# Kernel optimization log

Hardware: AMD Instinct MI355X
Metric: run time of the kernel (lower is better)

## Reference

```python
import jax, jax.numpy as jnp
import numpy as np

KNOTS = 17

def _buffers(dtype=jnp.float32):
    t = jnp.linspace(0.0, 3.0, KNOTS, dtype=dtype)
    dt = 3.0 / (KNOTS - 1)
    w = jnp.full((KNOTS,), 2.0 * dt, dtype=dtype).at[0].set(dt).at[-1].set(dt)
    phi = jnp.exp(-jnp.square(t) / 2.0)
    return t, phi, w * phi


def setup_inputs() -> dict:
    key = jax.random.key(0)
    k1, k2 = jax.random.split(key)
    T, B, D, P = 32, 64, 256, 1024
    proj = jax.random.normal(k1, (T, B, D), dtype=jnp.float32)
    A = jax.random.normal(k2, (D, P), dtype=jnp.float32)
    return {"proj": proj, "A": A}


def reference(proj, A):
    t, phi, weights = _buffers(proj.dtype)
    # column-normalize random projection directions (matches A.div_(norm.clamp_min))
    A = A / jnp.maximum(jnp.linalg.norm(A, axis=0, keepdims=True), 1e-12)
    B = proj.shape[-2]
    # (T, B, P) projections, broadcast against knots -> (T, B, P, K)
    x_t = (proj @ A)[..., None] * t
    # empirical characteristic function averaged over batch dim B (dim -3)
    cos_mean = jnp.cos(x_t).mean(axis=-3)  # (T, P, K)
    sin_mean = jnp.sin(x_t).mean(axis=-3)  # (T, P, K)
    err = jnp.square(cos_mean - phi) + jnp.square(sin_mean)
    statistic = (err @ weights) * B  # (T, P)
    return statistic.mean()
```

## Files before the change

kernel.cpp:

```cpp
#include <hip/hip_runtime.h>

#define T_DIM 32
#define B_DIM 64
#define D_DIM 256
#define P_DIM 1024
#define NK    17
#define DT    0.1875f
#define NBLK  512

__global__ __launch_bounds__(512) void sig_main_kernel(const float* __restrict__ proj,
                                                       const float* __restrict__ A,
                                                       float* __restrict__ partials) {
  __shared__ float smem[16384];
  const int tid  = threadIdx.x;
  const int lane = tid & 63;
  const int wave = tid >> 6;
  const int p0   = blockIdx.x * 64;
  const int t    = blockIdx.y;

  float4* s4 = (float4*)smem;
  float4* p4 = (float4*)(smem + 8192);

  float xacc[8];
#pragma unroll
  for (int j = 0; j < 8; ++j) xacc[j] = 0.f;
  float nacc = 0.f;

  const float4* Ag = (const float4*)(A + p0);
  const float4* Pg = (const float4*)(proj + (size_t)t * B_DIM * D_DIM);

  for (int dc = 0; dc < D_DIM; dc += 128) {
#pragma unroll
    for (int r = 0; r < 4; ++r) {
      int i = tid + r * 512;
      int da = i >> 4, ca = i & 15;
      s4[i] = Ag[(dc + da) * (P_DIM / 4) + ca];
      int bp = i >> 5, cp = i & 31;
      p4[i] = Pg[(size_t)bp * (D_DIM / 4) + dc / 4 + cp];
    }
    __syncthreads();

    const float4* prow = p4 + wave * 8 * 32;
#pragma unroll 2
    for (int ds4 = 0; ds4 < 32; ++ds4) {
      int dd = ds4 * 4;
      float a0 = smem[(dd + 0) * 64 + lane];
      float a1 = smem[(dd + 1) * 64 + lane];
      float a2 = smem[(dd + 2) * 64 + lane];
      float a3 = smem[(dd + 3) * 64 + lane];
      nacc = fmaf(a0, a0, nacc);
      nacc = fmaf(a1, a1, nacc);
      nacc = fmaf(a2, a2, nacc);
      nacc = fmaf(a3, a3, nacc);
#pragma unroll
      for (int j = 0; j < 8; ++j) {
        float4 pj = prow[j * 32 + ds4];
        xacc[j] = fmaf(pj.x, a0, xacc[j]);
        xacc[j] = fmaf(pj.y, a1, xacc[j]);
        xacc[j] = fmaf(pj.z, a2, xacc[j]);
        xacc[j] = fmaf(pj.w, a3, xacc[j]);
      }
    }
    __syncthreads();
  }

  const float inv = rsqrtf(fmaxf(nacc, 1e-24f));
  float cs[NK], ss[NK];
#pragma unroll
  for (int k = 1; k < NK; ++k) { cs[k] = 0.f; ss[k] = 0.f; }

#pragma unroll
  for (int j = 0; j < 8; ++j) {
    float th = xacc[j] * inv * DT;
    float s1, c1;
    __sincosf(th, &s1, &c1);
    float twoc = 2.f * c1;
    float ckm1 = 1.f, skm1 = 0.f;
    float ck = c1, sk = s1;
    cs[1] += c1;
    ss[1] += s1;
#pragma unroll
    for (int k = 2; k < NK; ++k) {
      float cn = fmaf(twoc, ck, -ckm1);
      float sn = fmaf(twoc, sk, -skm1);
      cs[k] += cn;
      ss[k] += sn;
      ckm1 = ck; skm1 = sk; ck = cn; sk = sn;
    }
  }

#pragma unroll
  for (int k = 1; k < NK; ++k) {
    int k1 = k - 1;
    smem[k1 * 512 + wave * 64 + lane]        = cs[k];
    smem[8192 + k1 * 512 + wave * 64 + lane] = ss[k];
  }
  __syncthreads();

  float part = 0.f;
#pragma unroll
  for (int r = 0; r < 2; ++r) {
    int e  = tid + r * 512;
    int k1 = e >> 6;
    int pl = e & 63;
    const float* bc = &smem[k1 * 512 + pl];
    const float* bs = &smem[8192 + k1 * 512 + pl];
    float C = 0.f, S = 0.f;
#pragma unroll
    for (int w = 0; w < 8; ++w) { C += bc[w * 64]; S += bs[w * 64]; }
    float cm  = C * (1.f / 64.f);
    float sm  = S * (1.f / 64.f);
    float tk  = (float)(k1 + 1) * DT;
    float phi = __expf(-0.5f * tk * tk);
    float wk  = ((k1 == NK - 2) ? DT : 2.f * DT) * phi;
    float dc  = cm - phi;
    part = fmaf(wk, fmaf(dc, dc, sm * sm), part);
  }
  part *= (1.f / 512.f);

#pragma unroll
  for (int off = 32; off > 0; off >>= 1)
    part += __shfl_down(part, off, 64);
  __syncthreads();
  if (lane == 0) smem[wave] = part;
  __syncthreads();
  if (tid == 0) {
    float s = 0.f;
#pragma unroll
    for (int w = 0; w < 8; ++w) s += smem[w];
    partials[blockIdx.y * 16 + blockIdx.x] = s;
  }
}

__global__ __launch_bounds__(256) void sig_finalize_kernel(const float* __restrict__ partials,
                                                           float* __restrict__ out) {
  __shared__ float red[4];
  const int tid  = threadIdx.x;
  const int lane = tid & 63;
  const int wave = tid >> 6;
  float v = partials[tid] + partials[tid + 256];
#pragma unroll
  for (int off = 32; off > 0; off >>= 1)
    v += __shfl_down(v, off, 64);
  if (lane == 0) red[wave] = v;
  __syncthreads();
  if (tid == 0) out[0] = red[0] + red[1] + red[2] + red[3];
}

extern "C" void kernel_launch(void* const* d_in, const int* in_sizes, int n_in,
                              void* d_out, int out_size, void* d_ws, size_t ws_size,
                              hipStream_t stream) {
  const float* proj = (const float*)d_in[0];
  const float* A    = (const float*)d_in[1];
  float* partials   = (float*)d_ws;
  float* out        = (float*)d_out;

  sig_main_kernel<<<dim3(16, 32), dim3(512), 0, stream>>>(proj, A, partials);
  sig_finalize_kernel<<<dim3(1), dim3(256), 0, stream>>>(partials, out);
}
```

Before: 86.39 us.

## Stage all of A in LDS once and stream proj via register double-buffering

The whole 256x64 tile of A is now loaded into shared memory in one pass, replacing the two chunked passes that also staged proj. Each wave reads its 8 proj rows straight from global memory as wave-uniform float4 loads, double-buffered in registers and prefetched two steps ahead, so the inner loop needs no LDS reads of proj and no barrier per chunk. The wave index is made scalar with readfirstlane, and launch bounds now request 4 blocks per CU. This adds register pressure from the 16 float4 prefetch buffers, and the launch-bounds hint may force the compiler to spill.

```diff
diff --git a/kernel.cpp b/kernel.cpp
--- a/kernel.cpp
+++ b/kernel.cpp
@@ -6,44 +6,45 @@
 #define P_DIM 1024
 #define NK    17
 #define DT    0.1875f
-#define NBLK  512
 
-__global__ __launch_bounds__(512) void sig_main_kernel(const float* __restrict__ proj,
-                                                       const float* __restrict__ A,
-                                                       float* __restrict__ partials) {
+__global__ __launch_bounds__(512, 4) void sig_main_kernel(const float* __restrict__ proj,
+                                                          const float* __restrict__ A,
+                                                          float* __restrict__ partials) {
   __shared__ float smem[16384];
   const int tid  = threadIdx.x;
   const int lane = tid & 63;
-  const int wave = tid >> 6;
   const int p0   = blockIdx.x * 64;
   const int t    = blockIdx.y;
+  const int wv   = __builtin_amdgcn_readfirstlane(tid >> 6);
 
-  float4* s4 = (float4*)smem;
-  float4* p4 = (float4*)(smem + 8192);
+  {
+    const float4* Ag = (const float4*)(A + p0);
+    float4* s4 = (float4*)smem;
+#pragma unroll
+    for (int r = 0; r < 8; ++r) {
+      int i = tid + r * 512;
+      int d = i >> 4, c = i & 15;
+      s4[i] = Ag[d * (P_DIM / 4) + c];
+    }
+  }
+  __syncthreads();
+
+  const float4* Pg = (const float4*)(proj + ((size_t)(t * B_DIM + wv * 8)) * D_DIM);
 
   float xacc[8];
 #pragma unroll
   for (int j = 0; j < 8; ++j) xacc[j] = 0.f;
   float nacc = 0.f;
 
-  const float4* Ag = (const float4*)(A + p0);
-  const float4* Pg = (const float4*)(proj + (size_t)t * B_DIM * D_DIM);
+  float4 pa[8], pb[8];
+#pragma unroll
+  for (int j = 0; j < 8; ++j) pa[j] = Pg[j * 64 + 0];
+#pragma unroll
+  for (int j = 0; j < 8; ++j) pb[j] = Pg[j * 64 + 1];
 
-  for (int dc = 0; dc < D_DIM; dc += 128) {
-#pragma unroll
-    for (int r = 0; r < 4; ++r) {
-      int i = tid + r * 512;
-      int da = i >> 4, ca = i & 15;
-      s4[i] = Ag[(dc + da) * (P_DIM / 4) + ca];
-      int bp = i >> 5, cp = i & 31;
-      p4[i] = Pg[(size_t)bp * (D_DIM / 4) + dc / 4 + cp];
-    }
-    __syncthreads();
-
-    const float4* prow = p4 + wave * 8 * 32;
-#pragma unroll 2
-    for (int ds4 = 0; ds4 < 32; ++ds4) {
-      int dd = ds4 * 4;
+  for (int g = 0; g < 64; g += 2) {
+    {
+      int dd = 4 * g;
       float a0 = smem[(dd + 0) * 64 + lane];
       float a1 = smem[(dd + 1) * 64 + lane];
       float a2 = smem[(dd + 2) * 64 + lane];
@@ -54,14 +55,40 @@
       nacc = fmaf(a3, a3, nacc);
 #pragma unroll
       for (int j = 0; j < 8; ++j) {
-        float4 pj = prow[j * 32 + ds4];
-        xacc[j] = fmaf(pj.x, a0, xacc[j]);
-        xacc[j] = fmaf(pj.y, a1, xacc[j]);
-        xacc[j] = fmaf(pj.z, a2, xacc[j]);
-        xacc[j] = fmaf(pj.w, a3, xacc[j]);
+        xacc[j] = fmaf(pa[j].x, a0, xacc[j]);
+        xacc[j] = fmaf(pa[j].y, a1, xacc[j]);
+        xacc[j] = fmaf(pa[j].z, a2, xacc[j]);
+        xacc[j] = fmaf(pa[j].w, a3, xacc[j]);
       }
     }
-    __syncthreads();
+    {
+      int gp = (g + 2 < 64) ? (g + 2) : 63;
+#pragma unroll
+      for (int j = 0; j < 8; ++j) pa[j] = Pg[j * 64 + gp];
+    }
+    {
+      int dd = 4 * g + 4;
+      float a0 = smem[(dd + 0) * 64 + lane];
+      float a1 = smem[(dd + 1) * 64 + lane];
+      float a2 = smem[(dd + 2) * 64 + lane];
+      float a3 = smem[(dd + 3) * 64 + lane];
+      nacc = fmaf(a0, a0, nacc);
+      nacc = fmaf(a1, a1, nacc);
+      nacc = fmaf(a2, a2, nacc);
+      nacc = fmaf(a3, a3, nacc);
+#pragma unroll
+      for (int j = 0; j < 8; ++j) {
+        xacc[j] = fmaf(pb[j].x, a0, xacc[j]);
+        xacc[j] = fmaf(pb[j].y, a1, xacc[j]);
+        xacc[j] = fmaf(pb[j].z, a2, xacc[j]);
+        xacc[j] = fmaf(pb[j].w, a3, xacc[j]);
+      }
+    }
+    {
+      int gp = (g + 3 < 64) ? (g + 3) : 63;
+#pragma unroll
+      for (int j = 0; j < 8; ++j) pb[j] = Pg[j * 64 + gp];
+    }
   }
 
   const float inv = rsqrtf(fmaxf(nacc, 1e-24f));
@@ -89,11 +116,12 @@
     }
   }
 
+  __syncthreads();
 #pragma unroll
   for (int k = 1; k < NK; ++k) {
     int k1 = k - 1;
-    smem[k1 * 512 + wave * 64 + lane]        = cs[k];
-    smem[8192 + k1 * 512 + wave * 64 + lane] = ss[k];
+    smem[k1 * 512 + wv * 64 + lane]        = cs[k];
+    smem[8192 + k1 * 512 + wv * 64 + lane] = ss[k];
   }
   __syncthreads();
 
@@ -122,7 +150,7 @@
   for (int off = 32; off > 0; off >>= 1)
     part += __shfl_down(part, off, 64);
   __syncthreads();
-  if (lane == 0) smem[wave] = part;
+  if (lane == 0) smem[wv] = part;
   __syncthreads();
   if (tid == 0) {
     float s = 0.f;
```

Measured after the change: 107.9 us. 1.25x slower.

## Use bf16 MFMA for projection GEMM with prep kernel for normalization and conversion

Applied to the files above, without the earlier changes.

Adds a prep kernel that computes the column norms of A, normalizes A, transposes it and converts it to bf16. The same kernel also converts proj to bf16. The main kernel then does the projection GEMM with 32x32x16 bf16 MFMA instructions instead of scalar FP32 FMAs, with 256-thread blocks and padded LDS rows. This aims to remove the FP32 ALU cost of the matmul, at the price of an extra kernel launch, extra global traffic, and bf16 rounding of the inputs, which changes the accuracy of the phase values fed to sin/cos.

```diff
diff --git a/kernel.cpp b/kernel.cpp
--- a/kernel.cpp
+++ b/kernel.cpp
@@ -6,115 +6,177 @@
 #define P_DIM 1024
 #define NK    17
 #define DT    0.1875f
-#define NBLK  512
-
-__global__ __launch_bounds__(512) void sig_main_kernel(const float* __restrict__ proj,
-                                                       const float* __restrict__ A,
+
+#define KC    128
+#define LROW  136
+#define PROW  264
+
+typedef __bf16 bf16x8 __attribute__((ext_vector_type(8)));
+typedef float  f32x16 __attribute__((ext_vector_type(16)));
+
+static __device__ __forceinline__ unsigned short f2bf(float f) {
+  unsigned u = __float_as_uint(f);
+  u += 0x7fffu + ((u >> 16) & 1u);
+  return (unsigned short)(u >> 16);
+}
+
+__global__ __launch_bounds__(256) void prep_kernel(const float* __restrict__ proj,
+                                                   const float* __restrict__ A,
+                                                   unsigned short* __restrict__ projbf,
+                                                   unsigned short* __restrict__ ATbf) {
+  const int tid = threadIdx.x;
+  if (blockIdx.x < 16) {
+    __shared__ unsigned short tile[64 * PROW];
+    __shared__ float red[4][64];
+    __shared__ float invn[64];
+    const int pl = tid & 63;
+    const int dq = tid >> 6;
+    const int p0 = blockIdx.x * 64;
+    const float* Ac = A + p0 + pl;
+    float s = 0.f;
+#pragma unroll 8
+    for (int i = 0; i < 64; ++i) {
+      float v = Ac[(size_t)(dq * 64 + i) * P_DIM];
+      s = fmaf(v, v, s);
+    }
+    red[dq][pl] = s;
+    __syncthreads();
+    if (tid < 64) {
+      float tot = red[0][pl] + red[1][pl] + red[2][pl] + red[3][pl];
+      invn[pl] = rsqrtf(fmaxf(tot, 1e-24f));
+    }
+    __syncthreads();
+    const float inv = invn[pl];
+#pragma unroll 8
+    for (int i = 0; i < 64; ++i) {
+      int d = dq * 64 + i;
+      float v = Ac[(size_t)d * P_DIM] * inv;
+      tile[pl * PROW + d] = f2bf(v);
+    }
+    __syncthreads();
+#pragma unroll
+    for (int r = 0; r < 8; ++r) {
+      int idx = tid + r * 256;
+      int row = idx >> 5, c = idx & 31;
+      uint4 v = *(const uint4*)&tile[row * PROW + c * 8];
+      *(uint4*)(ATbf + ((size_t)(p0 + row) * D_DIM + c * 8)) = v;
+    }
+  } else {
+    const int pb = blockIdx.x - 16;
+    const float4* src = (const float4*)proj + (size_t)pb * 2048;
+    unsigned short* dst = projbf + (size_t)pb * 8192;
+#pragma unroll
+    for (int r = 0; r < 8; ++r) {
+      int i = tid + r * 256;
+      float4 v = src[i];
+      ushort4 o;
+      o.x = f2bf(v.x); o.y = f2bf(v.y); o.z = f2bf(v.z); o.w = f2bf(v.w);
+      *(ushort4*)(dst + (size_t)i * 4) = o;
+    }
+  }
+}
+
+__global__ __launch_bounds__(256) void sig_main_kernel(const unsigned short* __restrict__ projbf,
+                                                       const unsigned short* __restrict__ ATbf,
                                                        float* __restrict__ partials) {
-  __shared__ float smem[16384];
+  __shared__ unsigned short sm[2 * 64 * LROW];
+  float* smf = (float*)sm;
   const int tid  = threadIdx.x;
   const int lane = tid & 63;
-  const int wave = tid >> 6;
+  const int wv   = tid >> 6;
   const int p0   = blockIdx.x * 64;
   const int t    = blockIdx.y;
 
-  float4* s4 = (float4*)smem;
-  float4* p4 = (float4*)(smem + 8192);
-
-  float xacc[8];
-#pragma unroll
-  for (int j = 0; j < 8; ++j) xacc[j] = 0.f;
-  float nacc = 0.f;
-
-  const float4* Ag = (const float4*)(A + p0);
-  const float4* Pg = (const float4*)(proj + (size_t)t * B_DIM * D_DIM);
-
-  for (int dc = 0; dc < D_DIM; dc += 128) {
+  unsigned short* sp = sm;
+  unsigned short* sa = sm + 64 * LROW;
+
+  const unsigned short* gp = projbf + (size_t)t * B_DIM * D_DIM;
+  const unsigned short* ga = ATbf + (size_t)p0 * D_DIM;
+
+  const int mt = wv >> 1, nt = wv & 1;
+  const int mrow = mt * 32 + (lane & 31);
+  const int nrow = nt * 32 + (lane & 31);
+  const int koff = (lane >> 5) * 8;
+
+  f32x16 acc = {0.f, 0.f, 0.f, 0.f, 0.f, 0.f, 0.f, 0.f,
+                0.f, 0.f, 0.f, 0.f, 0.f, 0.f, 0.f, 0.f};
+
+  for (int kc = 0; kc < D_DIM; kc += KC) {
 #pragma unroll
     for (int r = 0; r < 4; ++r) {
-      int i = tid + r * 512;
-      int da = i >> 4, ca = i & 15;
-      s4[i] = Ag[(dc + da) * (P_DIM / 4) + ca];
-      int bp = i >> 5, cp = i & 31;
-      p4[i] = Pg[(size_t)bp * (D_DIM / 4) + dc / 4 + cp];
-    }
-    __syncthreads();
-
-    const float4* prow = p4 + wave * 8 * 32;
-#pragma unroll 2
-    for (int ds4 = 0; ds4 < 32; ++ds4) {
-      int dd = ds4 * 4;
-      float a0 = smem[(dd + 0) * 64 + lane];
-      float a1 = smem[(dd + 1) * 64 + lane];
-      float a2 = smem[(dd + 2) * 64 + lane];
-      float a3 = smem[(dd + 3) * 64 + lane];
-      nacc = fmaf(a0, a0, nacc);
-      nacc = fmaf(a1, a1, nacc);
-      nacc = fmaf(a2, a2, nacc);
-      nacc = fmaf(a3, a3, nacc);
-#pragma unroll
-      for (int j = 0; j < 8; ++j) {
-        float4 pj = prow[j * 32 + ds4];
-        xacc[j] = fmaf(pj.x, a0, xacc[j]);
-        xacc[j] = fmaf(pj.y, a1, xacc[j]);
-        xacc[j] = fmaf(pj.z, a2, xacc[j]);
-        xacc[j] = fmaf(pj.w, a3, xacc[j]);
-      }
-    }
-    __syncthreads();
-  }
-
-  const float inv = rsqrtf(fmaxf(nacc, 1e-24f));
-  float cs[NK], ss[NK];
-#pragma unroll
-  for (int k = 1; k < NK; ++k) { cs[k] = 0.f; ss[k] = 0.f; }
-
-#pragma unroll
-  for (int j = 0; j < 8; ++j) {
-    float th = xacc[j] * inv * DT;
+      int idx = tid + r * 256;
+      int row = idx >> 4, c = idx & 15;
+      uint4 v = *(const uint4*)(gp + (size_t)row * D_DIM + kc + c * 8);
+      *(uint4*)&sp[row * LROW + c * 8] = v;
+      uint4 w = *(const uint4*)(ga + (size_t)row * D_DIM + kc + c * 8);
+      *(uint4*)&sa[row * LROW + c * 8] = w;
+    }
+    __syncthreads();
+
+#pragma unroll
+    for (int ks = 0; ks < 8; ++ks) {
+      int k = ks * 16 + koff;
+      bf16x8 af = *(const bf16x8*)&sp[mrow * LROW + k];
+      bf16x8 bf = *(const bf16x8*)&sa[nrow * LROW + k];
+      acc = __builtin_amdgcn_mfma_f32_32x32x16_bf16(af, bf, acc, 0, 0, 0);
+    }
+    __syncthreads();
+  }
+
+  float cs[NK - 1], ss[NK - 1];
+#pragma unroll
+  for (int k = 0; k < NK - 1; ++k) { cs[k] = 0.f; ss[k] = 0.f; }
+#pragma unroll
+  for (int r = 0; r < 16; ++r) {
+    float th = acc[r] * DT;
     float s1, c1;
     __sincosf(th, &s1, &c1);
     float twoc = 2.f * c1;
     float ckm1 = 1.f, skm1 = 0.f;
     float ck = c1, sk = s1;
-    cs[1] += c1;
-    ss[1] += s1;
+    cs[0] += c1;
+    ss[0] += s1;
 #pragma unroll
     for (int k = 2; k < NK; ++k) {
       float cn = fmaf(twoc, ck, -ckm1);
       float sn = fmaf(twoc, sk, -skm1);
-      cs[k] += cn;
-      ss[k] += sn;
+      cs[k - 1] += cn;
+      ss[k - 1] += sn;
       ckm1 = ck; skm1 = sk; ck = cn; sk = sn;
     }
   }
 
 #pragma unroll
-  for (int k = 1; k < NK; ++k) {
-    int k1 = k - 1;
-    smem[k1 * 512 + wave * 64 + lane]        = cs[k];
-    smem[8192 + k1 * 512 + wave * 64 + lane] = ss[k];
+  for (int k = 0; k < NK - 1; ++k) {
+    cs[k] += __shfl_xor(cs[k], 32, 64);
+    ss[k] += __shfl_xor(ss[k], 32, 64);
+  }
+
+  if (lane < 32) {
+    int p = nt * 32 + (lane & 31);
+#pragma unroll
+    for (int k = 0; k < NK - 1; ++k) {
+      smf[k * 128 + mt * 64 + p]        = cs[k];
+      smf[2048 + k * 128 + mt * 64 + p] = ss[k];
+    }
   }
   __syncthreads();
 
   float part = 0.f;
 #pragma unroll
-  for (int r = 0; r < 2; ++r) {
-    int e  = tid + r * 512;
+  for (int r = 0; r < 4; ++r) {
+    int e  = tid + r * 256;
     int k1 = e >> 6;
     int pl = e & 63;
-    const float* bc = &smem[k1 * 512 + pl];
-    const float* bs = &smem[8192 + k1 * 512 + pl];
-    float C = 0.f, S = 0.f;
-#pragma unroll
-    for (int w = 0; w < 8; ++w) { C += bc[w * 64]; S += bs[w * 64]; }
+    float C = smf[k1 * 128 + pl] + smf[k1 * 128 + 64 + pl];
+    float S = smf[2048 + k1 * 128 + pl] + smf[2048 + k1 * 128 + 64 + pl];
     float cm  = C * (1.f / 64.f);
-    float sm  = S * (1.f / 64.f);
+    float sm_ = S * (1.f / 64.f);
     float tk  = (float)(k1 + 1) * DT;
     float phi = __expf(-0.5f * tk * tk);
     float wk  = ((k1 == NK - 2) ? DT : 2.f * DT) * phi;
     float dc  = cm - phi;
-    part = fmaf(wk, fmaf(dc, dc, sm * sm), part);
+    part = fmaf(wk, fmaf(dc, dc, sm_ * sm_), part);
   }
   part *= (1.f / 512.f);
 
@@ -122,14 +184,10 @@
   for (int off = 32; off > 0; off >>= 1)
     part += __shfl_down(part, off, 64);
   __syncthreads();
-  if (lane == 0) smem[wave] = part;
-  __syncthreads();
-  if (tid == 0) {
-    float s = 0.f;
-#pragma unroll
-    for (int w = 0; w < 8; ++w) s += smem[w];
-    partials[blockIdx.y * 16 + blockIdx.x] = s;
-  }
+  if (lane == 0) smf[4096 + wv] = part;
+  __syncthreads();
+  if (tid == 0)
+    partials[blockIdx.y * 16 + blockIdx.x] = smf[4096] + smf[4097] + smf[4098] + smf[4099];
 }
 
 __global__ __launch_bounds__(256) void sig_finalize_kernel(const float* __restrict__ partials,
@@ -152,9 +210,13 @@
                               hipStream_t stream) {
   const float* proj = (const float*)d_in[0];
   const float* A    = (const float*)d_in[1];
-  float* partials   = (float*)d_ws;
   float* out        = (float*)d_out;
 
-  sig_main_kernel<<<dim3(16, 32), dim3(512), 0, stream>>>(proj, A, partials);
+  unsigned short* projbf = (unsigned short*)d_ws;
+  unsigned short* ATbf   = (unsigned short*)((char*)d_ws + 1536u * 1024);
+  float* partials        = (float*)((char*)d_ws + 2560u * 1024);
+
+  prep_kernel<<<dim3(80), dim3(256), 0, stream>>>(proj, A, projbf, ATbf);
+  sig_main_kernel<<<dim3(16, 32), dim3(256), 0, stream>>>(projbf, ATbf, partials);
   sig_finalize_kernel<<<dim3(1), dim3(256), 0, stream>>>(partials, out);
 }
```

New measurement: 72.26 us. -16.4%, faster.
